# Kernel tuning notes

Measured on AMD Instinct MI355X. Metric: run time of the kernel, lower is better.

The kernel has to match this reference:

```python
import jax, jax.numpy as jnp
import numpy as np

B, S, D = 4, 2048, 1024
H = 16
DH = D // H  # 64
THETA = 10000.0


def setup_inputs() -> dict:
    key = jax.random.key(0)
    ks = jax.random.split(key, 7)
    scale = 1.0 / np.sqrt(D)
    return {
        "Q": jax.random.normal(ks[0], (B, S, D), dtype=jnp.float32),
        "K": jax.random.normal(ks[1], (B, S, D), dtype=jnp.float32),
        "V": jax.random.normal(ks[2], (B, S, D), dtype=jnp.float32),
        "Wq": jax.random.normal(ks[3], (D, D), dtype=jnp.float32) * scale,
        "Wk": jax.random.normal(ks[4], (D, D), dtype=jnp.float32) * scale,
        "Wv": jax.random.normal(ks[5], (D, D), dtype=jnp.float32) * scale,
        "Wo": jax.random.normal(ks[6], (D, D), dtype=jnp.float32) * scale,
    }


def _rope_tables(seq_len, d_head, theta, dtype):
    inv_freq = 1.0 / theta ** (jnp.arange(0, d_head, 2, dtype=jnp.float32) / d_head)
    ang = jnp.arange(seq_len, dtype=jnp.float32)[:, None] * inv_freq[None, :]  # [S, DH/2]
    return jnp.sin(ang).astype(dtype), jnp.cos(ang).astype(dtype)


def _apply_rope(x, sin, cos):
    # x: [B, H, S, DH]; sin/cos: [S, DH/2] broadcast over B,H
    x1 = x[..., 0::2]
    x2 = x[..., 1::2]
    x1r = x1 * cos - x2 * sin
    x2r = x1 * sin + x2 * cos
    return jnp.stack([x1r, x2r], axis=-1).reshape(x.shape)


def reference(Q, K, V, Wq, Wk, Wv, Wo):
    seq_len = Q.shape[-2]
    q = Q @ Wq.T
    k = K @ Wk.T
    v = V @ Wv.T

    def split(x):  # [B, S, D] -> [B, H, S, DH]
        return x.reshape(x.shape[0], seq_len, H, DH).transpose(0, 2, 1, 3)

    qh, kh, vh = split(q), split(k), split(v)

    sin, cos = _rope_tables(seq_len, DH, THETA, qh.dtype)
    qh = _apply_rope(qh, sin, cos)
    kh = _apply_rope(kh, sin, cos)

    # attention in fp32 (matches original cast)
    qf = qh.astype(jnp.float32)
    kf = kh.astype(jnp.float32)
    vf = vh.astype(jnp.float32)
    scale = 1.0 / np.sqrt(DH)
    scores = jnp.einsum('bhqd,bhkd->bhqk', qf, kf) * scale
    causal = jnp.tril(jnp.ones((seq_len, seq_len), dtype=bool))
    scores = jnp.where(causal, scores, -jnp.inf)
    attn = jax.nn.softmax(scores, axis=-1)
    out_h = jnp.einsum('bhqk,bhkd->bhqd', attn, vf).astype(Q.dtype)

    out = out_h.transpose(0, 2, 1, 3).reshape(Q.shape[0], seq_len, D)
    return out @ Wo.T
```

## Files before the change

kernel.cpp:

```cpp
#include <hip/hip_runtime.h>
#include <hip/hip_bf16.h>
#include <cmath>

#define B_ 4
#define S_ 2048
#define D_ 1024
#define H_ 16
#define DH_ 64

typedef __bf16 bf16_t;
typedef __bf16 bf16x8 __attribute__((ext_vector_type(8)));
typedef __bf16 bf16x4 __attribute__((ext_vector_type(4)));
typedef float f32x4 __attribute__((ext_vector_type(4)));

static __device__ __forceinline__ f32x4 mfma16(bf16x8 a, bf16x8 b, f32x4 c) {
    return __builtin_amdgcn_mfma_f32_16x16x32_bf16(a, b, c, 0, 0, 0);
}

static __device__ __forceinline__ float fast_exp2(float x) {
#if __has_builtin(__builtin_amdgcn_exp2f)
    return __builtin_amdgcn_exp2f(x);
#else
    float r; asm("v_exp_f32 %0, %1" : "=v"(r) : "v"(x)); return r;
#endif
}

static __device__ __forceinline__ void glds16(const void* g, void* l) {
    __builtin_amdgcn_global_load_lds(
        (const __attribute__((address_space(1))) unsigned int*)g,
        (__attribute__((address_space(3))) unsigned int*)l, 16, 0, 0);
}

__global__ __launch_bounds__(256)
void prep_kernel(const float* __restrict__ Wq, const float* __restrict__ Wk,
                 const float* __restrict__ Wv, const float* __restrict__ Wo,
                 bf16_t* __restrict__ Wb, float2* __restrict__ tab)
{
    int bid = blockIdx.x;
    if (bid < 256) {
        int idx = bid * 256 + threadIdx.x;
        int s = idx >> 5, i = idx & 31;
        float inv = powf(10000.f, -(2.f * i) / 64.f);
        float ang = (float)s * inv;
        tab[idx] = make_float2(sinf(ang), cosf(ang));
    } else {
        int i = (bid - 256) * 256 + threadIdx.x;
        int t = i >> 17, j = i & 131071;
        const float* src = (t == 0) ? Wq : (t == 1) ? Wk : (t == 2) ? Wv : Wo;
        const float4* s = (const float4*)(src + (size_t)j * 8);
        float4 a = s[0], b = s[1];
        bf16x8 v = { (__bf16)a.x, (__bf16)a.y, (__bf16)a.z, (__bf16)a.w,
                     (__bf16)b.x, (__bf16)b.y, (__bf16)b.z, (__bf16)b.w };
        *(bf16x8*)(Wb + (size_t)i * 8) = v;
    }
}

template<int EPI>
__global__ __launch_bounds__(256)
void proj_kernel(const float* __restrict__ X, const bf16_t* __restrict__ W,
                 bf16_t* __restrict__ dst, const float2* __restrict__ tab)
{
    __shared__ bf16x8 lA[128 * 8];
    __shared__ bf16x8 lB[128 * 8];
    const int tid = threadIdx.x;
    const int gm0 = blockIdx.x * 128;
    const int gn0 = blockIdx.y * 128;
    const int wid = tid >> 6, lane = tid & 63;
    const int lr = lane & 15, lh = lane >> 4;
    const int wm = (wid >> 1) * 64, wn = (wid & 1) * 64;

    int arow[4], aslot[4];
    const float* abase[4];
    #pragma unroll
    for (int i = 0; i < 4; ++i) {
        int slot = i * 256 + tid;
        int row = slot >> 3, s = slot & 7, c = s ^ (row & 7);
        arow[i] = row; aslot[i] = s;
        abase[i] = X + (size_t)(gm0 + row) * D_ + c * 8;
    }
    float4 av0[4], av1[4];
    #pragma unroll
    for (int i = 0; i < 4; ++i) {
        av0[i] = *(const float4*)(abase[i]);
        av1[i] = *(const float4*)(abase[i] + 4);
    }

    f32x4 acc[4][4] = {};

    #pragma unroll 1
    for (int kt = 0; kt < D_ / 64; ++kt) {
        __syncthreads();
        #pragma unroll
        for (int i = 0; i < 4; ++i) {
            int base = wid * 64 + i * 256;
            int slot = base + lane;
            int row = slot >> 3, s = slot & 7, c = s ^ (row & 7);
            glds16(W + (size_t)(gn0 + row) * D_ + kt * 64 + c * 8, &lB[base]);
        }
        #pragma unroll
        for (int i = 0; i < 4; ++i) {
            lA[arow[i] * 8 + aslot[i]] = bf16x8{
                (__bf16)av0[i].x, (__bf16)av0[i].y, (__bf16)av0[i].z, (__bf16)av0[i].w,
                (__bf16)av1[i].x, (__bf16)av1[i].y, (__bf16)av1[i].z, (__bf16)av1[i].w };
        }
        __syncthreads();
        if (kt + 1 < D_ / 64) {
            #pragma unroll
            for (int i = 0; i < 4; ++i) {
                av0[i] = *(const float4*)(abase[i] + (kt + 1) * 64);
                av1[i] = *(const float4*)(abase[i] + (kt + 1) * 64 + 4);
            }
        }
        #pragma unroll
        for (int ks = 0; ks < 2; ++ks) {
            bf16x8 af[4], bfr[4];
            int kh = ks * 4 + lh;
            #pragma unroll
            for (int mi = 0; mi < 4; ++mi) { int r = wm + mi * 16 + lr; af[mi]  = lA[r * 8 + (kh ^ (r & 7))]; }
            #pragma unroll
            for (int ni = 0; ni < 4; ++ni) { int r = wn + ni * 16 + lr; bfr[ni] = lB[r * 8 + (kh ^ (r & 7))]; }
            #pragma unroll
            for (int mi = 0; mi < 4; ++mi)
                #pragma unroll
                for (int ni = 0; ni < 4; ++ni)
                    acc[mi][ni] = mfma16(af[mi], bfr[ni], acc[mi][ni]);
        }
    }

    #pragma unroll
    for (int mi = 0; mi < 4; ++mi) {
        #pragma unroll
        for (int j = 0; j < 4; ++j) {
            int m = gm0 + wm + mi * 16 + lh * 4 + j;
            int b = m >> 11, s = m & (S_ - 1);
            #pragma unroll
            for (int ni = 0; ni < 4; ++ni) {
                int n = gn0 + wn + ni * 16 + lr;
                int h = n >> 6, dh = n & 63;
                float x = acc[mi][ni][j];
                if (EPI == 0) {
                    float p = __shfl_xor(x, 1);
                    float2 sc = tab[s * 32 + (dh >> 1)];
                    float r = (dh & 1) ? (p * sc.x + x * sc.y)
                                       : (x * sc.y - p * sc.x);
                    dst[(((size_t)b * H_ + h) * S_ + s) * DH_ + dh] = (bf16_t)r;
                } else {
                    dst[(((size_t)b * H_ + h) * DH_ + dh) * S_ + s] = (bf16_t)x;
                }
            }
        }
    }
}

__global__ __launch_bounds__(256, 6)
void attn_kernel(const bf16_t* __restrict__ qh, const bf16_t* __restrict__ kh,
                 const bf16_t* __restrict__ vT, bf16_t* __restrict__ O)
{
    __shared__ bf16x8 lK[64 * 8];
    __shared__ bf16x8 lV[64 * 8];
    __shared__ bf16x8 lP8[4][128];
    const int tid = threadIdx.x, wid = tid >> 6, lane = tid & 63;
    const int lr = lane & 15, lh = lane >> 4;
    const int bh = blockIdx.x & 63;
    const int t  = 31 - (blockIdx.x >> 6);
    const bf16_t* Qp = qh + (size_t)bh * S_ * DH_;
    const bf16_t* Kp = kh + (size_t)bh * S_ * DH_;
    const bf16_t* Vp = vT + (size_t)bh * DH_ * S_;
    char* lP = (char*)lP8[wid];
    const int b = bh >> 4, h = bh & 15;
    const float QSCALE = 0.125f * 1.44269504f;
    const int wq = t * 64 + wid * 16;

    bf16x8 qf[2];
    #pragma unroll
    for (int ks = 0; ks < 2; ++ks) {
        bf16x8 q8 = *(const bf16x8*)(Qp + (size_t)(wq + lr) * DH_ + ks * 32 + lh * 8);
        #pragma unroll
        for (int e = 0; e < 8; ++e) q8[e] = (__bf16)((float)q8[e] * QSCALE);
        qf[ks] = q8;
    }

    f32x4 accO[4] = {};
    float mrun = -1e30f, lrun = 0.f;
    const int nkt = t + 1;

    #pragma unroll 1
    for (int kt = 0; kt < nkt; ++kt) {
        __syncthreads();
        #pragma unroll
        for (int i = 0; i < 2; ++i) {
            int base = i * 256 + (wid << 6);
            int slot = base + lane;
            int row = slot >> 3, s = slot & 7, c = s ^ (row & 7);
            glds16(Kp + (size_t)(kt * 64 + row) * DH_ + c * 8, &lK[base]);
            glds16(Vp + (size_t)row * S_ + kt * 64 + c * 8, &lV[base]);
        }
        __syncthreads();

        f32x4 sc[4] = {};
        __builtin_amdgcn_s_setprio(1);
        #pragma unroll
        for (int ks = 0; ks < 2; ++ks) {
            int kh8 = ks * 4 + lh;
            #pragma unroll
            for (int kvi = 0; kvi < 4; ++kvi) {
                int r = kvi * 16 + lr;
                bf16x8 kf = lK[r * 8 + (kh8 ^ (r & 7))];
                sc[kvi] = mfma16(kf, qf[ks], sc[kvi]);
            }
        }
        __builtin_amdgcn_s_setprio(0);

        const int kvb = kt * 64 + 4 * lh;
        const int qg = wq + lr;
        float pv[16];
        if (kt == t) {
            #pragma unroll
            for (int kvi = 0; kvi < 4; ++kvi)
                #pragma unroll
                for (int j = 0; j < 4; ++j) {
                    float x = sc[kvi][j];
                    if ((kvb + kvi * 16 + j) > qg) x = -1e30f;
                    pv[kvi * 4 + j] = x;
                }
        } else {
            #pragma unroll
            for (int kvi = 0; kvi < 4; ++kvi)
                #pragma unroll
                for (int j = 0; j < 4; ++j) pv[kvi * 4 + j] = sc[kvi][j];
        }

        float t0 = fmaxf(fmaxf(pv[0],  pv[1]),  pv[2]);
        float t1 = fmaxf(fmaxf(pv[3],  pv[4]),  pv[5]);
        float t2 = fmaxf(fmaxf(pv[6],  pv[7]),  pv[8]);
        float t3 = fmaxf(fmaxf(pv[9],  pv[10]), pv[11]);
        float t4 = fmaxf(fmaxf(pv[12], pv[13]), pv[14]);
        float u0 = fmaxf(fmaxf(t0, t1), t2);
        float u1 = fmaxf(fmaxf(t3, t4), pv[15]);
        float mxp = fmaxf(u0, u1);

        float mnew = mrun;
        bool skip = __all(mxp <= mrun + 8.0f);
        if (!skip) {
            float mx = fmaxf(mxp, __shfl_xor(mxp, 16));
            mx = fmaxf(mx, __shfl_xor(mx, 32));
            mnew = fmaxf(mrun, mx);
            float rs = fast_exp2(mrun - mnew);
            mrun = mnew;
            lrun *= rs;
            #pragma unroll
            for (int j = 0; j < 4; ++j) {
                float rj = __shfl(rs, 4 * lh + j);
                #pragma unroll
                for (int ni = 0; ni < 4; ++ni) accO[ni][j] *= rj;
            }
        }
        #pragma unroll
        for (int i = 0; i < 16; ++i) pv[i] = fast_exp2(pv[i] - mnew);
        float s8[8], s4v[4];
        #pragma unroll
        for (int i = 0; i < 8; ++i) s8[i] = pv[i] + pv[i + 8];
        #pragma unroll
        for (int i = 0; i < 4; ++i) s4v[i] = s8[i] + s8[i + 4];
        lrun += (s4v[0] + s4v[1]) + (s4v[2] + s4v[3]);

        #pragma unroll
        for (int kvi = 0; kvi < 4; ++kvi) {
            bf16x4 hv = { (__bf16)pv[kvi * 4 + 0], (__bf16)pv[kvi * 4 + 1],
                          (__bf16)pv[kvi * 4 + 2], (__bf16)pv[kvi * 4 + 3] };
            int slot = 2 * kvi + (lh >> 1);
            *(bf16x4*)(lP + lr * 128 + ((slot ^ (lr & 7)) * 16) + (lh & 1) * 8) = hv;
        }

        __builtin_amdgcn_s_setprio(1);
        #pragma unroll
        for (int ks = 0; ks < 2; ++ks) {
            int kh8 = ks * 4 + lh;
            int slot = 4 * ks + lh;
            bf16x8 pf = *(const bf16x8*)(lP + lr * 128 + ((slot ^ (lr & 7)) * 16));
            #pragma unroll
            for (int ni = 0; ni < 4; ++ni) {
                int r = ni * 16 + lr;
                bf16x8 vf = lV[r * 8 + (kh8 ^ (r & 7))];
                accO[ni] = mfma16(pf, vf, accO[ni]);
            }
        }
        __builtin_amdgcn_s_setprio(0);
    }

    lrun += __shfl_xor(lrun, 16);
    lrun += __shfl_xor(lrun, 32);

    #pragma unroll
    for (int j = 0; j < 4; ++j) {
        int s = wq + 4 * lh + j;
        float inv = 1.f / __shfl(lrun, 4 * lh + j);
        #pragma unroll
        for (int ni = 0; ni < 4; ++ni) {
            int dh = ni * 16 + lr;
            O[((size_t)(b * S_ + s)) * D_ + h * DH_ + dh] = (bf16_t)(accO[ni][j] * inv);
        }
    }
}

__global__ __launch_bounds__(256)
void out_kernel(const bf16_t* __restrict__ A, const bf16_t* __restrict__ W,
                float* __restrict__ out)
{
    __shared__ bf16x8 lA[128 * 8];
    __shared__ bf16x8 lB[128 * 8];
    const int tid = threadIdx.x;
    const int gm0 = blockIdx.x * 128;
    const int gn0 = blockIdx.y * 128;
    const int wid = tid >> 6, lane = tid & 63;
    const int lr = lane & 15, lh = lane >> 4;
    const int wm = (wid >> 1) * 64, wn = (wid & 1) * 64;

    f32x4 acc[4][4] = {};

    for (int kt = 0; kt < D_ / 64; ++kt) {
        const int k0 = kt * 64;
        __syncthreads();
        #pragma unroll
        for (int i = 0; i < 4; ++i) {
            int base = wid * 64 + i * 256;
            int slot = base + lane;
            int row = slot >> 3, s = slot & 7, c = s ^ (row & 7);
            glds16(A + (size_t)(gm0 + row) * D_ + k0 + c * 8, &lA[base]);
            glds16(W + (size_t)(gn0 + row) * D_ + k0 + c * 8, &lB[base]);
        }
        __syncthreads();
        #pragma unroll
        for (int ks = 0; ks < 2; ++ks) {
            bf16x8 af[4], bfr[4];
            int kh = ks * 4 + lh;
            #pragma unroll
            for (int mi = 0; mi < 4; ++mi) { int r = wm + mi * 16 + lr; af[mi]  = lA[r * 8 + (kh ^ (r & 7))]; }
            #pragma unroll
            for (int ni = 0; ni < 4; ++ni) { int r = wn + ni * 16 + lr; bfr[ni] = lB[r * 8 + (kh ^ (r & 7))]; }
            #pragma unroll
            for (int mi = 0; mi < 4; ++mi)
                #pragma unroll
                for (int ni = 0; ni < 4; ++ni)
                    acc[mi][ni] = mfma16(af[mi], bfr[ni], acc[mi][ni]);
        }
    }

    #pragma unroll
    for (int mi = 0; mi < 4; ++mi)
        #pragma unroll
        for (int j = 0; j < 4; ++j) {
            int m = gm0 + wm + mi * 16 + lh * 4 + j;
            #pragma unroll
            for (int ni = 0; ni < 4; ++ni) {
                int n = gn0 + wn + ni * 16 + lr;
                out[(size_t)m * D_ + n] = acc[mi][ni][j];
            }
        }
}

extern "C" void kernel_launch(void* const* d_in, const int* in_sizes, int n_in,
                              void* d_out, int out_size, void* d_ws, size_t ws_size,
                              hipStream_t stream)
{
    const float* Q  = (const float*)d_in[0];
    const float* K  = (const float*)d_in[1];
    const float* V  = (const float*)d_in[2];
    const float* Wq = (const float*)d_in[3];
    const float* Wk = (const float*)d_in[4];
    const float* Wv = (const float*)d_in[5];
    const float* Wo = (const float*)d_in[6];
    float* out = (float*)d_out;

    char* ws = (char*)d_ws;
    const size_t MB = 1024 * 1024;
    bf16_t* qh  = (bf16_t*)(ws);
    bf16_t* khb = (bf16_t*)(ws + 16 * MB);
    bf16_t* vT  = (bf16_t*)(ws + 32 * MB);
    bf16_t* Ob  = (bf16_t*)(ws + 48 * MB);
    bf16_t* Wb  = (bf16_t*)(ws + 64 * MB);
    float2* tab = (float2*)(ws + 72 * MB);

    prep_kernel<<<2304, 256, 0, stream>>>(Wq, Wk, Wv, Wo, Wb, tab);

    dim3 g(64, 8);
    proj_kernel<0><<<g, 256, 0, stream>>>(Q, Wb + 0 * 1048576, qh, tab);
    proj_kernel<0><<<g, 256, 0, stream>>>(K, Wb + 1 * 1048576, khb, tab);
    proj_kernel<1><<<g, 256, 0, stream>>>(V, Wb + 2 * 1048576, vT, tab);

    attn_kernel<<<2048, 256, 0, stream>>>(qh, khb, vT, Ob);

    out_kernel<<<g, 256, 0, stream>>>(Ob, Wb + 3 * 1048576, out);
}
```

Before: 180.5 us.

## Batch QKV projections into one launch and double-buffer K/V tiles in attention

Merges the three separate projection launches into a single grid with a z dimension that selects input, weight and epilogue per slice. This cuts launch overhead and fills the GPU with one larger grid, which matters because each projection alone is only 512 blocks. The attention kernel now double-buffers K/V tiles in LDS, prefetching the next tile while the current one is computed, and replaces two barriers per iteration with one. LDS use doubles and the occupancy hint drops from 6 to 4 blocks per CU, which may reduce latency hiding.

Result: slower. 208.8 us (+15.7%).

```diff
diff --git a/kernel.cpp b/kernel.cpp
--- a/kernel.cpp
+++ b/kernel.cpp
@@ -55,13 +55,20 @@
     }
 }
 
-template<int EPI>
 __global__ __launch_bounds__(256)
-void proj_kernel(const float* __restrict__ X, const bf16_t* __restrict__ W,
-                 bf16_t* __restrict__ dst, const float2* __restrict__ tab)
+void proj3_kernel(const float* __restrict__ Qi, const float* __restrict__ Ki,
+                  const float* __restrict__ Vi, const bf16_t* __restrict__ Wb,
+                  bf16_t* __restrict__ qh, bf16_t* __restrict__ kh,
+                  bf16_t* __restrict__ vT, const float2* __restrict__ tab)
 {
     __shared__ bf16x8 lA[128 * 8];
     __shared__ bf16x8 lB[128 * 8];
+    const int z = blockIdx.z;
+    const float* X = (z == 0) ? Qi : (z == 1) ? Ki : Vi;
+    const bf16_t* W = Wb + (size_t)z * 1048576;
+    bf16_t* dst = (z == 0) ? qh : (z == 1) ? kh : vT;
+    const int epi = (z == 2) ? 1 : 0;
+
     const int tid = threadIdx.x;
     const int gm0 = blockIdx.x * 128;
     const int gn0 = blockIdx.y * 128;
@@ -114,11 +121,11 @@
         #pragma unroll
         for (int ks = 0; ks < 2; ++ks) {
             bf16x8 af[4], bfr[4];
-            int kh = ks * 4 + lh;
-            #pragma unroll
-            for (int mi = 0; mi < 4; ++mi) { int r = wm + mi * 16 + lr; af[mi]  = lA[r * 8 + (kh ^ (r & 7))]; }
-            #pragma unroll
-            for (int ni = 0; ni < 4; ++ni) { int r = wn + ni * 16 + lr; bfr[ni] = lB[r * 8 + (kh ^ (r & 7))]; }
+            int kh8 = ks * 4 + lh;
+            #pragma unroll
+            for (int mi = 0; mi < 4; ++mi) { int r = wm + mi * 16 + lr; af[mi]  = lA[r * 8 + (kh8 ^ (r & 7))]; }
+            #pragma unroll
+            for (int ni = 0; ni < 4; ++ni) { int r = wn + ni * 16 + lr; bfr[ni] = lB[r * 8 + (kh8 ^ (r & 7))]; }
             #pragma unroll
             for (int mi = 0; mi < 4; ++mi)
                 #pragma unroll
@@ -138,7 +145,7 @@
                 int n = gn0 + wn + ni * 16 + lr;
                 int h = n >> 6, dh = n & 63;
                 float x = acc[mi][ni][j];
-                if (EPI == 0) {
+                if (epi == 0) {
                     float p = __shfl_xor(x, 1);
                     float2 sc = tab[s * 32 + (dh >> 1)];
                     float r = (dh & 1) ? (p * sc.x + x * sc.y)
@@ -152,12 +159,12 @@
     }
 }
 
-__global__ __launch_bounds__(256, 6)
+__global__ __launch_bounds__(256, 4)
 void attn_kernel(const bf16_t* __restrict__ qh, const bf16_t* __restrict__ kh,
                  const bf16_t* __restrict__ vT, bf16_t* __restrict__ O)
 {
-    __shared__ bf16x8 lK[64 * 8];
-    __shared__ bf16x8 lV[64 * 8];
+    __shared__ bf16x8 lK[2][64 * 8];
+    __shared__ bf16x8 lV[2][64 * 8];
     __shared__ bf16x8 lP8[4][128];
     const int tid = threadIdx.x, wid = tid >> 6, lane = tid & 63;
     const int lr = lane & 15, lh = lane >> 4;
@@ -171,6 +178,17 @@
     const float QSCALE = 0.125f * 1.44269504f;
     const int wq = t * 64 + wid * 16;
 
+    const bf16_t* kga[2]; const bf16_t* vga[2]; int sbase[2];
+    #pragma unroll
+    for (int i = 0; i < 2; ++i) {
+        int base = i * 256 + (wid << 6);
+        int slot = base + lane;
+        int row = slot >> 3, s = slot & 7, c = s ^ (row & 7);
+        sbase[i] = base;
+        kga[i] = Kp + (size_t)row * DH_ + c * 8;
+        vga[i] = Vp + (size_t)row * S_ + c * 8;
+    }
+
     bf16x8 qf[2];
     #pragma unroll
     for (int ks = 0; ks < 2; ++ks) {
@@ -184,18 +202,23 @@
     float mrun = -1e30f, lrun = 0.f;
     const int nkt = t + 1;
 
+    #pragma unroll
+    for (int i = 0; i < 2; ++i) {
+        glds16(kga[i], &lK[0][sbase[i]]);
+        glds16(vga[i], &lV[0][sbase[i]]);
+    }
+    __syncthreads();
+    int cur = 0;
+
     #pragma unroll 1
     for (int kt = 0; kt < nkt; ++kt) {
-        __syncthreads();
-        #pragma unroll
-        for (int i = 0; i < 2; ++i) {
-            int base = i * 256 + (wid << 6);
-            int slot = base + lane;
-            int row = slot >> 3, s = slot & 7, c = s ^ (row & 7);
-            glds16(Kp + (size_t)(kt * 64 + row) * DH_ + c * 8, &lK[base]);
-            glds16(Vp + (size_t)row * S_ + kt * 64 + c * 8, &lV[base]);
-        }
-        __syncthreads();
+        if (kt + 1 < nkt) {
+            #pragma unroll
+            for (int i = 0; i < 2; ++i) {
+                glds16(kga[i] + (size_t)(kt + 1) * 64 * DH_, &lK[cur ^ 1][sbase[i]]);
+                glds16(vga[i] + (size_t)(kt + 1) * 64,       &lV[cur ^ 1][sbase[i]]);
+            }
+        }
 
         f32x4 sc[4] = {};
         __builtin_amdgcn_s_setprio(1);
@@ -205,7 +228,7 @@
             #pragma unroll
             for (int kvi = 0; kvi < 4; ++kvi) {
                 int r = kvi * 16 + lr;
-                bf16x8 kf = lK[r * 8 + (kh8 ^ (r & 7))];
+                bf16x8 kf = lK[cur][r * 8 + (kh8 ^ (r & 7))];
                 sc[kvi] = mfma16(kf, qf[ks], sc[kvi]);
             }
         }
@@ -281,11 +304,14 @@
             #pragma unroll
             for (int ni = 0; ni < 4; ++ni) {
                 int r = ni * 16 + lr;
-                bf16x8 vf = lV[r * 8 + (kh8 ^ (r & 7))];
+                bf16x8 vf = lV[cur][r * 8 + (kh8 ^ (r & 7))];
                 accO[ni] = mfma16(pf, vf, accO[ni]);
             }
         }
         __builtin_amdgcn_s_setprio(0);
+
+        __syncthreads();
+        cur ^= 1;
     }
 
     lrun += __shfl_xor(lrun, 16);
@@ -382,13 +408,7 @@
     float2* tab = (float2*)(ws + 72 * MB);
 
     prep_kernel<<<2304, 256, 0, stream>>>(Wq, Wk, Wv, Wo, Wb, tab);
-
-    dim3 g(64, 8);
-    proj_kernel<0><<<g, 256, 0, stream>>>(Q, Wb + 0 * 1048576, qh, tab);
-    proj_kernel<0><<<g, 256, 0, stream>>>(K, Wb + 1 * 1048576, khb, tab);
-    proj_kernel<1><<<g, 256, 0, stream>>>(V, Wb + 2 * 1048576, vT, tab);
-
+    proj3_kernel<<<dim3(64, 8, 3), 256, 0, stream>>>(Q, K, V, Wb, qh, khb, vT, tab);
     attn_kernel<<<2048, 256, 0, stream>>>(qh, khb, vT, Ob);
-
-    out_kernel<<<g, 256, 0, stream>>>(Ob, Wb + 3 * 1048576, out);
-}
+    out_kernel<<<dim3(64, 8), 256, 0, stream>>>(Ob, Wb + 3 * 1048576, out);
+}
```
